# Optimization experiments

Hardware: AMD Instinct MI355X
Metric: run time of the kernel (lower is better)

## Reference

```python
import jax, jax.numpy as jnp
import numpy as np

N, T = 8192, 8192
RB, CB = 64, 64  # row_blocks, col_blocks
HID = 3          # hidden_upper from mar_small_config


def _partition_ids(total, nblocks, rng):
    # mirrors: ones + multinomial(remaining), every block >= 1
    part = np.ones(nblocks, dtype=np.int64)
    part += rng.multinomial(total - nblocks, [1.0 / nblocks] * nblocks)
    return np.repeat(np.arange(nblocks), part).astype(np.int32)


def setup_inputs() -> dict:
    key = jax.random.key(0)
    ks = jax.random.split(key, 4)
    rng = np.random.default_rng(42)
    X = jax.random.normal(ks[0], (N, T), dtype=jnp.float32)
    row_ids = jnp.asarray(_partition_ids(N, RB, rng))  # [N] sorted block ids
    col_ids = jnp.asarray(_partition_ids(T, CB, rng))  # [T] sorted block ids
    W1 = jax.random.normal(ks[1], (1, HID), dtype=jnp.float32)
    b1 = jnp.zeros((HID,), jnp.float32)
    W2 = jax.random.normal(ks[2], (HID, HID), dtype=jnp.float32)
    b2 = jnp.zeros((HID,), jnp.float32)
    W3 = jax.random.normal(ks[3], (HID, 1), dtype=jnp.float32)
    b3 = jnp.zeros((1,), jnp.float32)
    return {"X": X, "row_ids": row_ids, "col_ids": col_ids,
            "W1": W1, "b1": b1, "W2": W2, "b2": b2, "W3": W3, "b3": b3}


def _block_mean(X, row_ids, col_ids):
    # fused segment-reduce replacing the O(RB*CB) python loop + .item() syncs
    row_counts = jax.ops.segment_sum(jnp.ones((N,), X.dtype), row_ids, num_segments=RB)
    col_counts = jax.ops.segment_sum(jnp.ones((T,), X.dtype), col_ids, num_segments=CB)
    s = jax.ops.segment_sum(X, row_ids, num_segments=RB)        # [RB, T]
    s = jax.ops.segment_sum(s.T, col_ids, num_segments=CB).T    # [RB, CB]
    return s / (row_counts[:, None] * col_counts[None, :]), row_counts, col_counts


def _mar_generator(x_small, W1, b1, W2, b2, W3, b3):
    # small per-cell relu MLP -> sigmoid propensity (stand-in for MAR_missingness)
    h = x_small[..., None]                    # [RB, CB, 1]
    h = jax.nn.relu(h @ W1 + b1)
    h = jax.nn.relu(h @ W2 + b2)
    return jax.nn.sigmoid((h @ W3 + b3)[..., 0])  # [RB, CB]


def reference(X, row_ids, col_ids, W1, b1, W2, b2, W3, b3):
    x_small, row_counts, col_counts = _block_mean(X, row_ids, col_ids)
    propensity = _mar_generator(x_small, W1, b1, W2, b2, W3, b3)
    row_cumsum = jnp.concatenate([jnp.zeros((1,), jnp.int32),
                                  jnp.cumsum(row_counts.astype(jnp.int32))])
    col_cumsum = jnp.concatenate([jnp.zeros((1,), jnp.int32),
                                  jnp.cumsum(col_counts.astype(jnp.int32))])
    return propensity, row_cumsum, col_cumsum
```

## Files before the change

kernel.cpp:

```cpp
#include <hip/hip_runtime.h>
#include <math.h>

#define NROWS 8192
#define NCOLS 8192
#define RB 64
#define CB 64

__global__ __launch_bounds__(256) void fused_blocksum_kernel(
    const float* __restrict__ X,
    const int*   __restrict__ row_ids,
    const int*   __restrict__ col_ids,
    float*       __restrict__ acc_g,
    float*       __restrict__ cnts,
    float*       __restrict__ out)
{
    __shared__ int   rids[64];
    __shared__ float lacc[64];
    __shared__ int   hist[64];

    const int tid = threadIdx.x;
    const int bx  = blockIdx.x & 7;
    const int by  = blockIdx.x >> 3;

    if (blockIdx.x < 2) {
        const int* ids = (blockIdx.x == 0) ? row_ids : col_ids;
        if (tid < 64) hist[tid] = 0;
        __syncthreads();
        for (int i = tid; i < NROWS; i += 256)
            atomicAdd(&hist[ids[i]], 1);
        __syncthreads();
        if (tid < 64) cnts[blockIdx.x * 64 + tid] = (float)hist[tid];
        if (tid == 0) {
            float* obase = out + RB * CB + blockIdx.x * (RB + 1);
            int c = 0;
            obase[0] = 0.0f;
            for (int i = 0; i < 64; ++i) { c += hist[i]; obase[i + 1] = (float)c; }
        }
        __syncthreads();
    }

    if (tid < 64) {
        rids[tid] = row_ids[by * 64 + tid];
        lacc[tid] = 0.0f;
    }
    __syncthreads();

    const int c = bx * 1024 + tid * 4;
    const int4 cb4 = *(const int4*)(col_ids + c);
    const float* Xp = X + (size_t)by * 64 * NCOLS + c;

    float4 a = make_float4(0.f, 0.f, 0.f, 0.f);
    int cur = rids[0];

    #pragma unroll 4
    for (int i = 0; i < 64; ++i) {
        const int rb = rids[i];
        if (rb != cur) {
            atomicAdd(&lacc[cb4.x], a.x);
            atomicAdd(&lacc[cb4.y], a.y);
            atomicAdd(&lacc[cb4.z], a.z);
            atomicAdd(&lacc[cb4.w], a.w);
            __syncthreads();
            if (tid < 64 && lacc[tid] != 0.0f)
                atomicAdd(&acc_g[cur * 64 + tid], lacc[tid]);
            __syncthreads();
            if (tid < 64) lacc[tid] = 0.0f;
            __syncthreads();
            a = make_float4(0.f, 0.f, 0.f, 0.f);
            cur = rb;
        }
        const float4 v = *(const float4*)(Xp + (size_t)i * NCOLS);
        a.x += v.x; a.y += v.y; a.z += v.z; a.w += v.w;
    }
    atomicAdd(&lacc[cb4.x], a.x);
    atomicAdd(&lacc[cb4.y], a.y);
    atomicAdd(&lacc[cb4.z], a.z);
    atomicAdd(&lacc[cb4.w], a.w);
    __syncthreads();
    if (tid < 64 && lacc[tid] != 0.0f)
        atomicAdd(&acc_g[cur * 64 + tid], lacc[tid]);
}

__global__ __launch_bounds__(256) void mlp_kernel(
    const float* __restrict__ acc_g,
    const float* __restrict__ cnts,
    const float* __restrict__ W1, const float* __restrict__ b1,
    const float* __restrict__ W2, const float* __restrict__ b2,
    const float* __restrict__ W3, const float* __restrict__ b3,
    float*       __restrict__ out)
{
    const int cell = blockIdx.x * 256 + threadIdx.x;
    const int rb = cell >> 6, cb = cell & 63;
    const float mean = acc_g[cell] / (cnts[rb] * cnts[64 + cb]);

    float h1[3], h2[3];
    #pragma unroll
    for (int j = 0; j < 3; ++j)
        h1[j] = fmaxf(mean * W1[j] + b1[j], 0.f);
    #pragma unroll
    for (int j = 0; j < 3; ++j) {
        float v = b2[j];
        #pragma unroll
        for (int i = 0; i < 3; ++i) v += h1[i] * W2[i * 3 + j];
        h2[j] = fmaxf(v, 0.f);
    }
    float z = b3[0];
    #pragma unroll
    for (int i = 0; i < 3; ++i) z += h2[i] * W3[i];

    out[cell] = 1.0f / (1.0f + expf(-z));
}

extern "C" void kernel_launch(void* const* d_in, const int* in_sizes, int n_in,
                              void* d_out, int out_size, void* d_ws, size_t ws_size,
                              hipStream_t stream) {
    const float* X       = (const float*)d_in[0];
    const int*   row_ids = (const int*)  d_in[1];
    const int*   col_ids = (const int*)  d_in[2];
    const float* W1      = (const float*)d_in[3];
    const float* b1      = (const float*)d_in[4];
    const float* W2      = (const float*)d_in[5];
    const float* b2      = (const float*)d_in[6];
    const float* W3      = (const float*)d_in[7];
    const float* b3      = (const float*)d_in[8];
    float* out = (float*)d_out;

    float* acc_g = (float*)d_ws;
    float* cnts  = acc_g + RB * CB;

    hipMemsetAsync(d_ws, 0, (RB * CB + 128) * sizeof(float), stream);

    fused_blocksum_kernel<<<1024, 256, 0, stream>>>(X, row_ids, col_ids,
                                                    acc_g, cnts, out);
    mlp_kernel<<<16, 256, 0, stream>>>(acc_g, cnts,
                                       W1, b1, W2, b2, W3, b3, out);
}
```

Baseline: 387.3 us.

## Fuse MLP into block-sum kernel via last-block ticket and batch row loads

Merges the separate MLP kernel into the block-sum kernel: a global atomic ticket picks the last block to finish, which then computes the sigmoid propensity for all cells. The row loop is restructured into groups of 8 rows; when a group stays in one row block, its eight loads are issued unconditionally, giving more loads in flight. Threads whose four columns share a column block do one shared atomic instead of four. The intent is to remove one kernel launch and to raise memory-level parallelism, at the cost of a serial tail where one block processes all 4096 cells, and reliance on threadfence ordering.

Result: slower. 430.0 us (+11.0%).

```diff
diff --git a/kernel.cpp b/kernel.cpp
--- a/kernel.cpp
+++ b/kernel.cpp
@@ -5,18 +5,24 @@
 #define NCOLS 8192
 #define RB 64
 #define CB 64
+#define GRID 1024
 
-__global__ __launch_bounds__(256) void fused_blocksum_kernel(
+__global__ __launch_bounds__(256) void fused_kernel(
     const float* __restrict__ X,
     const int*   __restrict__ row_ids,
     const int*   __restrict__ col_ids,
     float*       __restrict__ acc_g,
     float*       __restrict__ cnts,
+    int*         __restrict__ ticket,
+    const float* __restrict__ W1, const float* __restrict__ b1,
+    const float* __restrict__ W2, const float* __restrict__ b2,
+    const float* __restrict__ W3, const float* __restrict__ b3,
     float*       __restrict__ out)
 {
     __shared__ int   rids[64];
     __shared__ float lacc[64];
     __shared__ int   hist[64];
+    __shared__ int   lastflag;
 
     const int tid = threadIdx.x;
     const int bx  = blockIdx.x & 7;
@@ -24,10 +30,10 @@
 
     if (blockIdx.x < 2) {
         const int* ids = (blockIdx.x == 0) ? row_ids : col_ids;
+        const int  n   = (blockIdx.x == 0) ? NROWS : NCOLS;
         if (tid < 64) hist[tid] = 0;
         __syncthreads();
-        for (int i = tid; i < NROWS; i += 256)
-            atomicAdd(&hist[ids[i]], 1);
+        for (int i = tid; i < n; i += 256) atomicAdd(&hist[ids[i]], 1);
         __syncthreads();
         if (tid < 64) cnts[blockIdx.x * 64 + tid] = (float)hist[tid];
         if (tid == 0) {
@@ -39,76 +45,89 @@
         __syncthreads();
     }
 
-    if (tid < 64) {
-        rids[tid] = row_ids[by * 64 + tid];
-        lacc[tid] = 0.0f;
+    if (tid < 64) { rids[tid] = row_ids[by * 64 + tid]; lacc[tid] = 0.0f; }
+    __syncthreads();
+
+    const int   c     = bx * 1024 + tid * 4;
+    const int4  cb4   = *(const int4*)(col_ids + c);
+    const bool  split = (cb4.x != cb4.w);
+    const float* Xp   = X + (size_t)(by * 64) * NCOLS + c;
+
+    float4 a  = make_float4(0.f, 0.f, 0.f, 0.f);
+    int    cur = rids[0];
+
+    auto FLUSH = [&](int blk) {
+        if (split) {
+            atomicAdd(&lacc[cb4.x], a.x); atomicAdd(&lacc[cb4.y], a.y);
+            atomicAdd(&lacc[cb4.z], a.z); atomicAdd(&lacc[cb4.w], a.w);
+        } else {
+            atomicAdd(&lacc[cb4.x], a.x + a.y + a.z + a.w);
+        }
+        __syncthreads();
+        if (tid < 64) {
+            const float v = lacc[tid];
+            if (v != 0.0f) atomicAdd(&acc_g[blk * 64 + tid], v);
+        }
+        __syncthreads();
+        if (tid < 64) lacc[tid] = 0.0f;
+        __syncthreads();
+        a = make_float4(0.f, 0.f, 0.f, 0.f);
+    };
+
+    #pragma unroll
+    for (int g = 0; g < 8; ++g) {
+        const int rb0 = rids[g * 8];
+        if (rb0 != cur) { FLUSH(cur); cur = rb0; }
+        if (rids[g * 8 + 7] == rb0) {
+            #pragma unroll
+            for (int j = 0; j < 8; ++j) {
+                const float4 v = *(const float4*)(Xp + (size_t)(g * 8 + j) * NCOLS);
+                a.x += v.x; a.y += v.y; a.z += v.z; a.w += v.w;
+            }
+        } else {
+            for (int j = 0; j < 8; ++j) {
+                const int rb = rids[g * 8 + j];
+                if (rb != cur) { FLUSH(cur); cur = rb; }
+                const float4 v = *(const float4*)(Xp + (size_t)(g * 8 + j) * NCOLS);
+                a.x += v.x; a.y += v.y; a.z += v.z; a.w += v.w;
+            }
+        }
+    }
+    FLUSH(cur);
+
+    if (tid == 0) {
+        __threadfence();
+        lastflag = (atomicAdd(ticket, 1) == GRID - 1);
     }
     __syncthreads();
+    if (lastflag) {
+        __threadfence();
+        float w1[3], bb1[3], w2[9], bb2[3], w3[3];
+        #pragma unroll
+        for (int i = 0; i < 3; ++i) { w1[i] = W1[i]; bb1[i] = b1[i]; bb2[i] = b2[i]; w3[i] = W3[i]; }
+        #pragma unroll
+        for (int i = 0; i < 9; ++i) w2[i] = W2[i];
+        const float bb3 = b3[0];
 
-    const int c = bx * 1024 + tid * 4;
-    const int4 cb4 = *(const int4*)(col_ids + c);
-    const float* Xp = X + (size_t)by * 64 * NCOLS + c;
-
-    float4 a = make_float4(0.f, 0.f, 0.f, 0.f);
-    int cur = rids[0];
-
-    #pragma unroll 4
-    for (int i = 0; i < 64; ++i) {
-        const int rb = rids[i];
-        if (rb != cur) {
-            atomicAdd(&lacc[cb4.x], a.x);
-            atomicAdd(&lacc[cb4.y], a.y);
-            atomicAdd(&lacc[cb4.z], a.z);
-            atomicAdd(&lacc[cb4.w], a.w);
-            __syncthreads();
-            if (tid < 64 && lacc[tid] != 0.0f)
-                atomicAdd(&acc_g[cur * 64 + tid], lacc[tid]);
-            __syncthreads();
-            if (tid < 64) lacc[tid] = 0.0f;
-            __syncthreads();
-            a = make_float4(0.f, 0.f, 0.f, 0.f);
-            cur = rb;
+        for (int cell = tid; cell < RB * CB; cell += 256) {
+            const int rb = cell >> 6, cb = cell & 63;
+            const float mean = acc_g[cell] / (cnts[rb] * cnts[64 + cb]);
+            float h1[3], h2[3];
+            #pragma unroll
+            for (int j = 0; j < 3; ++j) h1[j] = fmaxf(mean * w1[j] + bb1[j], 0.f);
+            #pragma unroll
+            for (int j = 0; j < 3; ++j) {
+                float v = bb2[j];
+                #pragma unroll
+                for (int i = 0; i < 3; ++i) v += h1[i] * w2[i * 3 + j];
+                h2[j] = fmaxf(v, 0.f);
+            }
+            float z = bb3;
+            #pragma unroll
+            for (int i = 0; i < 3; ++i) z += h2[i] * w3[i];
+            out[cell] = 1.0f / (1.0f + expf(-z));
         }
-        const float4 v = *(const float4*)(Xp + (size_t)i * NCOLS);
-        a.x += v.x; a.y += v.y; a.z += v.z; a.w += v.w;
     }
-    atomicAdd(&lacc[cb4.x], a.x);
-    atomicAdd(&lacc[cb4.y], a.y);
-    atomicAdd(&lacc[cb4.z], a.z);
-    atomicAdd(&lacc[cb4.w], a.w);
-    __syncthreads();
-    if (tid < 64 && lacc[tid] != 0.0f)
-        atomicAdd(&acc_g[cur * 64 + tid], lacc[tid]);
-}
-
-__global__ __launch_bounds__(256) void mlp_kernel(
-    const float* __restrict__ acc_g,
-    const float* __restrict__ cnts,
-    const float* __restrict__ W1, const float* __restrict__ b1,
-    const float* __restrict__ W2, const float* __restrict__ b2,
-    const float* __restrict__ W3, const float* __restrict__ b3,
-    float*       __restrict__ out)
-{
-    const int cell = blockIdx.x * 256 + threadIdx.x;
-    const int rb = cell >> 6, cb = cell & 63;
-    const float mean = acc_g[cell] / (cnts[rb] * cnts[64 + cb]);
-
-    float h1[3], h2[3];
-    #pragma unroll
-    for (int j = 0; j < 3; ++j)
-        h1[j] = fmaxf(mean * W1[j] + b1[j], 0.f);
-    #pragma unroll
-    for (int j = 0; j < 3; ++j) {
-        float v = b2[j];
-        #pragma unroll
-        for (int i = 0; i < 3; ++i) v += h1[i] * W2[i * 3 + j];
-        h2[j] = fmaxf(v, 0.f);
-    }
-    float z = b3[0];
-    #pragma unroll
-    for (int i = 0; i < 3; ++i) z += h2[i] * W3[i];
-
-    out[cell] = 1.0f / (1.0f + expf(-z));
 }
 
 extern "C" void kernel_launch(void* const* d_in, const int* in_sizes, int n_in,
@@ -125,13 +144,13 @@
     const float* b3      = (const float*)d_in[8];
     float* out = (float*)d_out;
 
-    float* acc_g = (float*)d_ws;
-    float* cnts  = acc_g + RB * CB;
+    float* acc_g  = (float*)d_ws;
+    float* cnts   = acc_g + RB * CB;
+    int*   ticket = (int*)(cnts + 128);
 
-    hipMemsetAsync(d_ws, 0, (RB * CB + 128) * sizeof(float), stream);
+    hipMemsetAsync(d_ws, 0, (RB * CB + 128 + 16) * sizeof(float), stream);
 
-    fused_blocksum_kernel<<<1024, 256, 0, stream>>>(X, row_ids, col_ids,
-                                                    acc_g, cnts, out);
-    mlp_kernel<<<16, 256, 0, stream>>>(acc_g, cnts,
-                                       W1, b1, W2, b2, W3, b3, out);
+    fused_kernel<<<GRID, 256, 0, stream>>>(X, row_ids, col_ids,
+                                           acc_g, cnts, ticket,
+                                           W1, b1, W2, b2, W3, b3, out);
 }
```
